# Kernel tuning notes

Measured on AMD Instinct MI355X. Metric: run time of the kernel, lower is better.

## Reference

```python
import jax, jax.numpy as jnp
import numpy as np

B, CIN, H, W = 16, 3, 128, 128
C = 256          # out_channels
NH = 8           # num_heads
HD = C // NH     # head_dim = 32
SCALE = HD ** -0.5
EPS = 1e-5


def setup_inputs() -> dict:
    key = jax.random.key(0)
    ks = jax.random.split(key, 8)
    def xavier(k, fan_out, fan_in):
        lim = np.sqrt(6.0 / (fan_in + fan_out))
        return jax.random.uniform(k, (fan_out, fan_in), jnp.float32, -lim, lim)
    return {
        "x": jax.random.normal(ks[0], (B, CIN, H, W), jnp.float32),
        "Wi": xavier(ks[1], C, CIN),      # input_conv 1x1
        "bi": jnp.zeros((C,), jnp.float32),
        "Wqkv": xavier(ks[2], 3 * C, C),  # qkv_conv 1x1, no bias
        "Wo": xavier(ks[3], C, C),        # output_proj
        "bo": jnp.zeros((C,), jnp.float32),
        "Wf": xavier(ks[4], C, C),        # feature_update_conv
        "bf": jnp.zeros((C,), jnp.float32),
        "gamma": jnp.ones((C,), jnp.float32),
        "beta": jnp.zeros((C,), jnp.float32),
        "rmean": jnp.zeros((C,), jnp.float32),
        "rvar": jnp.ones((C,), jnp.float32),
    }


def reference(x, Wi, bi, Wqkv, Wo, bo, Wf, bf, gamma, beta, rmean, rvar):
    b, _, h, w = x.shape
    hw = h * w
    # input 1x1 conv
    x1 = jnp.einsum('oi,bihw->bohw', Wi, x) + bi[:, None, None]
    # qkv 1x1 conv, reshape (b, NH, 3, HD, h*w) matching torch channel layout
    qkv = jnp.einsum('oi,bihw->bohw', Wqkv, x1).reshape(b, NH, 3, HD, hw)
    q, k, v = qkv[:, :, 0], qkv[:, :, 1], qkv[:, :, 2]  # each (b, NH, HD, hw)
    # channel-channel attention: (b, NH, HD, HD), sigmoid gate (no softmax)
    attention = jax.nn.sigmoid(jnp.einsum('bndp,bnep->bnde', q, k) * SCALE)
    A = jnp.einsum('bnde,bnep->bndp', attention, v).reshape(b, C, h, w)
    A = jnp.einsum('oi,bihw->bohw', Wo, A) + bo[:, None, None]
    A = jnp.einsum('oi,bihw->bohw', Wf, A) + bf[:, None, None]
    # BatchNorm2d (eval mode: running stats)
    inv = gamma / jnp.sqrt(rvar + EPS)
    A = (A - rmean[:, None, None]) * inv[:, None, None] + beta[:, None, None]
    A = jax.nn.silu(A)  # dropout is identity in eval
    out = A + x1
    return (out, attention)
```

## Files before the change

kernel.cpp:

```cpp
#include <hip/hip_runtime.h>
#include <math.h>


#define HW 16384
#define NBATCH 16
static constexpr float SCALE_ = 0.17677669529663687f;
static constexpr float EPS_ = 1e-5f;

#define WS_PART 0
#define WS_WFO  4096
#define WS_BFO  69632
#define WS_WB4  69888
#define WS_AQ   71168
#define WS_GG   76800

__device__ __forceinline__ float sigmoidf_(float z) {
  return 1.0f / (1.0f + __expf(-z));
}

__global__ __launch_bounds__(256) void k_prep(
    const float* __restrict__ x,
    const float* __restrict__ Wi, const float* __restrict__ bi,
    const float* __restrict__ Wqkv,
    const float* __restrict__ Wo, const float* __restrict__ bo,
    const float* __restrict__ Wf, const float* __restrict__ bf,
    float* __restrict__ part, float* __restrict__ Wfo,
    float* __restrict__ bfo, float* __restrict__ Wb4,
    float* __restrict__ aqg)
{
  const int bx = blockIdx.x;
  const int tid = threadIdx.x;
  if (bx < 256) {
    const int b = bx >> 4;
    const int pi = bx & 15;
    const int p0 = pi * 1024 + tid * 4;
    const float4 a0 = *reinterpret_cast<const float4*>(x + (size_t)(b * 3 + 0) * HW + p0);
    const float4 a1 = *reinterpret_cast<const float4*>(x + (size_t)(b * 3 + 1) * HW + p0);
    const float4 a2 = *reinterpret_cast<const float4*>(x + (size_t)(b * 3 + 2) * HW + p0);
    float v[9];
    v[0] = a0.x * a0.x + a0.y * a0.y + a0.z * a0.z + a0.w * a0.w;
    v[1] = a0.x * a1.x + a0.y * a1.y + a0.z * a1.z + a0.w * a1.w;
    v[2] = a0.x * a2.x + a0.y * a2.y + a0.z * a2.z + a0.w * a2.w;
    v[3] = a1.x * a1.x + a1.y * a1.y + a1.z * a1.z + a1.w * a1.w;
    v[4] = a1.x * a2.x + a1.y * a2.y + a1.z * a2.z + a1.w * a2.w;
    v[5] = a2.x * a2.x + a2.y * a2.y + a2.z * a2.z + a2.w * a2.w;
    v[6] = a0.x + a0.y + a0.z + a0.w;
    v[7] = a1.x + a1.y + a1.z + a1.w;
    v[8] = a2.x + a2.y + a2.z + a2.w;
    __shared__ float wred[4][9];
    const int lane = tid & 63, wid = tid >> 6;
#pragma unroll
    for (int k = 0; k < 9; ++k) {
      float s = v[k];
#pragma unroll
      for (int off = 32; off; off >>= 1) s += __shfl_down(s, off, 64);
      if (lane == 0) wred[wid][k] = s;
    }
    __syncthreads();
    if (tid < 9) {
      part[bx * 9 + tid] = wred[0][tid] + wred[1][tid] + wred[2][tid] + wred[3][tid];
    }
  } else if (bx < 512) {
    const int o = bx - 256;
    const float* wfr = Wf + (size_t)o * 256;
    const int i = tid;
    float acc = 0.f;
#pragma unroll 8
    for (int k = 0; k < 256; ++k) acc = fmaf(wfr[k], Wo[(size_t)k * 256 + i], acc);
    Wfo[(size_t)o * 256 + i] = acc;
  } else if (bx == 512) {
    Wb4[tid * 4 + 0] = Wi[tid * 3 + 0];
    Wb4[tid * 4 + 1] = Wi[tid * 3 + 1];
    Wb4[tid * 4 + 2] = Wi[tid * 3 + 2];
    Wb4[tid * 4 + 3] = bi[tid];
    float acc = bf[tid];
    const float* wfr = Wf + (size_t)tid * 256;
#pragma unroll 8
    for (int k = 0; k < 256; ++k) acc = fmaf(wfr[k], bo[k], acc);
    bfo[tid] = acc;
  } else {
    const int blk = bx - 513;
    const int rl = tid >> 2;
    const int ch = tid & 3;
    const int row = blk * 64 + rl;
    const float* wr = Wqkv + (size_t)row * 256 + ch * 64;
    float c0 = 0, c1 = 0, c2 = 0, c3 = 0;
#pragma unroll 8
    for (int c = 0; c < 64; ++c) {
      const float w = wr[c];
      const int cc = ch * 64 + c;
      c0 = fmaf(w, Wi[cc * 3 + 0], c0);
      c1 = fmaf(w, Wi[cc * 3 + 1], c1);
      c2 = fmaf(w, Wi[cc * 3 + 2], c2);
      c3 = fmaf(w, bi[cc], c3);
    }
    __shared__ float red[64][4][4];
    red[rl][ch][0] = c0; red[rl][ch][1] = c1;
    red[rl][ch][2] = c2; red[rl][ch][3] = c3;
    __syncthreads();
    const int j = tid & 3;
    aqg[(size_t)(blk * 64 + rl) * 4 + j] =
        red[rl][0][j] + red[rl][1][j] + red[rl][2][j] + red[rl][3][j];
  }
}

__global__ __launch_bounds__(1024) void k_solve(
    const float* __restrict__ part, const float* __restrict__ aqg,
    const float* __restrict__ Wfo, const float* __restrict__ bfo,
    const float* __restrict__ gamma, const float* __restrict__ beta,
    const float* __restrict__ rmean, const float* __restrict__ rvar,
    float* __restrict__ att_out,
    float* __restrict__ Gg)
{
  const int b = blockIdx.x;
  const int tid = threadIdx.x;
  __shared__ float Ms[9];
  __shared__ float aq[768][5];
  __shared__ float att_s[8][32][33];
  __shared__ float4 A4[256];
  __shared__ float4 redv[256][4];

  if (tid < 9) {
    float s = 0.f;
    for (int j = 0; j < 16; ++j) s += part[(b * 16 + j) * 9 + tid];
    Ms[tid] = s;
  }
  for (int i = tid; i < 3072; i += 1024) aq[i >> 2][i & 3] = aqg[i];
  __syncthreads();
  const float M00 = Ms[0], M01 = Ms[1], M02 = Ms[2], M11 = Ms[3], M12 = Ms[4], M22 = Ms[5];
  const float s0 = Ms[6], s1 = Ms[7], s2 = Ms[8];
  for (int idx = tid; idx < 8192; idx += 1024) {
    const int n = idx >> 10, r = idx & 1023, d = r >> 5, e = r & 31;
    const float* q = aq[n * 96 + d];
    const float* k = aq[n * 96 + 32 + e];
    const float q0 = q[0], q1 = q[1], q2 = q[2], q3 = q[3];
    const float k0 = k[0], k1 = k[1], k2 = k[2], k3 = k[3];
    const float t = q0 * (M00 * k0 + M01 * k1 + M02 * k2)
                  + q1 * (M01 * k0 + M11 * k1 + M12 * k2)
                  + q2 * (M02 * k0 + M12 * k1 + M22 * k2)
                  + q3 * (s0 * k0 + s1 * k1 + s2 * k2)
                  + k3 * (s0 * q0 + s1 * q1 + s2 * q2)
                  + 16384.0f * q3 * k3;
    const float a = sigmoidf_(SCALE_ * t);
    att_s[n][d][e] = a;
    att_out[b * 8192 + idx] = a;
  }
  __syncthreads();
  {
    const int c = tid >> 2, j = tid & 3;
    const int n = c >> 5, d = c & 31;
    float acc = 0.f;
    const float* arow = att_s[n][d];
#pragma unroll 8
    for (int e = 0; e < 32; ++e) acc = fmaf(arow[e], aq[n * 96 + 64 + e][j], acc);
    ((float*)&A4[c])[j] = acc;
  }
  __syncthreads();
  {
    const int o = tid >> 2, ch = tid & 3;
    const float* wr = Wfo + (size_t)o * 256 + ch * 64;
    float a0 = 0, a1 = 0, a2 = 0, a3 = 0;
#pragma unroll 8
    for (int i = 0; i < 64; ++i) {
      const float w = wr[i];
      const float4 av = A4[ch * 64 + i];
      a0 = fmaf(w, av.x, a0);
      a1 = fmaf(w, av.y, a1);
      a2 = fmaf(w, av.z, a2);
      a3 = fmaf(w, av.w, a3);
    }
    redv[o][ch] = make_float4(a0, a1, a2, a3);
  }
  __syncthreads();
  {
    const int o = tid >> 2, j = tid & 3;
    float acc = ((const float*)&redv[o][0])[j] + ((const float*)&redv[o][1])[j]
              + ((const float*)&redv[o][2])[j] + ((const float*)&redv[o][3])[j];
    if (j == 3) acc += bfo[o];
    const float inv = gamma[o] / sqrtf(rvar[o] + EPS_);
    float outv;
    if (j == 3) outv = (acc - rmean[o]) * inv + beta[o];
    else        outv = acc * inv;
    Gg[(size_t)(b * 256 + o) * 4 + j] = outv;
  }
}

__global__ __launch_bounds__(256) void k_final(
    const float* __restrict__ x,
    const float4* __restrict__ Gg4,
    const float4* __restrict__ Wb4,
    float* __restrict__ out)
{
  const int b = blockIdx.z;
  const int c0 = blockIdx.y * 32;
  const int tid = threadIdx.x;
  const int p4 = (blockIdx.x * 256 + tid) * 4;
  __shared__ float4 sg[32], sw[32];
  if (tid < 32) sg[tid] = Gg4[b * 256 + c0 + tid];
  else if (tid < 64) sw[tid - 32] = Wb4[c0 + tid - 32];
  __syncthreads();
  const float4 X0 = *reinterpret_cast<const float4*>(x + (size_t)(b * 3 + 0) * HW + p4);
  const float4 X1 = *reinterpret_cast<const float4*>(x + (size_t)(b * 3 + 1) * HW + p4);
  const float4 X2 = *reinterpret_cast<const float4*>(x + (size_t)(b * 3 + 2) * HW + p4);
  float* ob = out + (size_t)(b * 256 + c0) * HW + p4;
#pragma unroll 2
  for (int ci = 0; ci < 32; ++ci) {
    const float4 g = sg[ci];
    const float4 w = sw[ci];
    float4 r;
    {
      const float y = fmaf(g.x, X0.x, fmaf(g.y, X1.x, fmaf(g.z, X2.x, g.w)));
      const float sil = y * sigmoidf_(y);
      r.x = sil + fmaf(w.x, X0.x, fmaf(w.y, X1.x, fmaf(w.z, X2.x, w.w)));
    }
    {
      const float y = fmaf(g.x, X0.y, fmaf(g.y, X1.y, fmaf(g.z, X2.y, g.w)));
      const float sil = y * sigmoidf_(y);
      r.y = sil + fmaf(w.x, X0.y, fmaf(w.y, X1.y, fmaf(w.z, X2.y, w.w)));
    }
    {
      const float y = fmaf(g.x, X0.z, fmaf(g.y, X1.z, fmaf(g.z, X2.z, g.w)));
      const float sil = y * sigmoidf_(y);
      r.z = sil + fmaf(w.x, X0.z, fmaf(w.y, X1.z, fmaf(w.z, X2.z, w.w)));
    }
    {
      const float y = fmaf(g.x, X0.w, fmaf(g.y, X1.w, fmaf(g.z, X2.w, g.w)));
      const float sil = y * sigmoidf_(y);
      r.w = sil + fmaf(w.x, X0.w, fmaf(w.y, X1.w, fmaf(w.z, X2.w, w.w)));
    }
    *reinterpret_cast<float4*>(ob) = r;
    ob += HW;
  }
}

extern "C" void kernel_launch(void* const* d_in, const int* in_sizes, int n_in,
                              void* d_out, int out_size, void* d_ws, size_t ws_size,
                              hipStream_t stream) {
  const float* x     = (const float*)d_in[0];
  const float* Wi    = (const float*)d_in[1];
  const float* bi    = (const float*)d_in[2];
  const float* Wqkv  = (const float*)d_in[3];
  const float* Wo    = (const float*)d_in[4];
  const float* bo    = (const float*)d_in[5];
  const float* Wf    = (const float*)d_in[6];
  const float* bf    = (const float*)d_in[7];
  const float* gamma = (const float*)d_in[8];
  const float* beta  = (const float*)d_in[9];
  const float* rmean = (const float*)d_in[10];
  const float* rvar  = (const float*)d_in[11];

  float* out = (float*)d_out;
  float* att = out + (size_t)NBATCH * 256 * HW;
  float* wsf = (float*)d_ws;

  k_prep<<<dim3(525), dim3(256), 0, stream>>>(x, Wi, bi, Wqkv, Wo, bo, Wf, bf,
                                              wsf + WS_PART, wsf + WS_WFO,
                                              wsf + WS_BFO, wsf + WS_WB4,
                                              wsf + WS_AQ);
  k_solve<<<dim3(NBATCH), dim3(1024), 0, stream>>>(wsf + WS_PART, wsf + WS_AQ,
                                                   wsf + WS_WFO, wsf + WS_BFO,
                                                   gamma, beta, rmean, rvar,
                                                   att, wsf + WS_GG);
  k_final<<<dim3(16, 8, NBATCH), dim3(256), 0, stream>>>(
      x, (const float4*)(wsf + WS_GG), (const float4*)(wsf + WS_WB4), out);
}
```

Before: 80.49 us.

## Split solve kernel per head and fuse output projection into final kernel

Replaces the 16-block per-batch solve kernel with a per-(head,batch) kernel that computes the sigmoid channel attention and attention·v. The Wfo projection, bias and batchnorm folding move into the prologue of the final elementwise kernel, computed per 32-channel slice. This spreads the serial solve stage across many more CUs to cut its latency. In exchange, every final block redundantly loads a 32x256 Wfo slice and does a small reduction before streaming output. Some prep-loop unroll factors are also raised.

```diff
diff --git a/kernel.cpp b/kernel.cpp
--- a/kernel.cpp
+++ b/kernel.cpp
@@ -12,7 +12,7 @@
 #define WS_BFO  69632
 #define WS_WB4  69888
 #define WS_AQ   71168
-#define WS_GG   76800
+#define WS_A4G  75776
 
 __device__ __forceinline__ float sigmoidf_(float z) {
   return 1.0f / (1.0f + __expf(-z));
@@ -65,7 +65,7 @@
     const float* wfr = Wf + (size_t)o * 256;
     const int i = tid;
     float acc = 0.f;
-#pragma unroll 8
+#pragma unroll 32
     for (int k = 0; k < 256; ++k) acc = fmaf(wfr[k], Wo[(size_t)k * 256 + i], acc);
     Wfo[(size_t)o * 256 + i] = acc;
   } else if (bx == 512) {
@@ -75,7 +75,7 @@
     Wb4[tid * 4 + 3] = bi[tid];
     float acc = bf[tid];
     const float* wfr = Wf + (size_t)tid * 256;
-#pragma unroll 8
+#pragma unroll 16
     for (int k = 0; k < 256; ++k) acc = fmaf(wfr[k], bo[k], acc);
     bfo[tid] = acc;
   } else {
@@ -104,35 +104,35 @@
   }
 }
 
-__global__ __launch_bounds__(1024) void k_solve(
+__global__ __launch_bounds__(256) void k_solveA(
     const float* __restrict__ part, const float* __restrict__ aqg,
-    const float* __restrict__ Wfo, const float* __restrict__ bfo,
-    const float* __restrict__ gamma, const float* __restrict__ beta,
-    const float* __restrict__ rmean, const float* __restrict__ rvar,
     float* __restrict__ att_out,
-    float* __restrict__ Gg)
+    float* __restrict__ A4g)
 {
-  const int b = blockIdx.x;
+  const int n = blockIdx.x;
+  const int b = blockIdx.y;
   const int tid = threadIdx.x;
   __shared__ float Ms[9];
-  __shared__ float aq[768][5];
-  __shared__ float att_s[8][32][33];
-  __shared__ float4 A4[256];
-  __shared__ float4 redv[256][4];
-
+  __shared__ float aqh[96][5];
+  __shared__ float att_s[32][33];
   if (tid < 9) {
     float s = 0.f;
     for (int j = 0; j < 16; ++j) s += part[(b * 16 + j) * 9 + tid];
     Ms[tid] = s;
   }
-  for (int i = tid; i < 3072; i += 1024) aq[i >> 2][i & 3] = aqg[i];
+  if (tid < 96) {
+    const float4 v = *reinterpret_cast<const float4*>(aqg + (size_t)(n * 96 + tid) * 4);
+    aqh[tid][0] = v.x; aqh[tid][1] = v.y; aqh[tid][2] = v.z; aqh[tid][3] = v.w;
+  }
   __syncthreads();
   const float M00 = Ms[0], M01 = Ms[1], M02 = Ms[2], M11 = Ms[3], M12 = Ms[4], M22 = Ms[5];
   const float s0 = Ms[6], s1 = Ms[7], s2 = Ms[8];
-  for (int idx = tid; idx < 8192; idx += 1024) {
-    const int n = idx >> 10, r = idx & 1023, d = r >> 5, e = r & 31;
-    const float* q = aq[n * 96 + d];
-    const float* k = aq[n * 96 + 32 + e];
+#pragma unroll
+  for (int r = 0; r < 4; ++r) {
+    const int idx = tid + r * 256;
+    const int d = idx >> 5, e = idx & 31;
+    const float* q = aqh[d];
+    const float* k = aqh[32 + e];
     const float q0 = q[0], q1 = q[1], q2 = q[2], q3 = q[3];
     const float k0 = k[0], k1 = k[1], k2 = k[2], k3 = k[3];
     const float t = q0 * (M00 * k0 + M01 * k1 + M02 * k2)
@@ -142,91 +142,101 @@
                   + k3 * (s0 * q0 + s1 * q1 + s2 * q2)
                   + 16384.0f * q3 * k3;
     const float a = sigmoidf_(SCALE_ * t);
-    att_s[n][d][e] = a;
-    att_out[b * 8192 + idx] = a;
-  }
-  __syncthreads();
-  {
-    const int c = tid >> 2, j = tid & 3;
-    const int n = c >> 5, d = c & 31;
+    att_s[d][e] = a;
+    att_out[(size_t)(b * 8 + n) * 1024 + idx] = a;
+  }
+  __syncthreads();
+  if (tid < 128) {
+    const int d = tid >> 2, j = tid & 3;
     float acc = 0.f;
-    const float* arow = att_s[n][d];
 #pragma unroll 8
-    for (int e = 0; e < 32; ++e) acc = fmaf(arow[e], aq[n * 96 + 64 + e][j], acc);
-    ((float*)&A4[c])[j] = acc;
-  }
-  __syncthreads();
-  {
-    const int o = tid >> 2, ch = tid & 3;
-    const float* wr = Wfo + (size_t)o * 256 + ch * 64;
-    float a0 = 0, a1 = 0, a2 = 0, a3 = 0;
-#pragma unroll 8
-    for (int i = 0; i < 64; ++i) {
-      const float w = wr[i];
-      const float4 av = A4[ch * 64 + i];
-      a0 = fmaf(w, av.x, a0);
-      a1 = fmaf(w, av.y, a1);
-      a2 = fmaf(w, av.z, a2);
-      a3 = fmaf(w, av.w, a3);
-    }
-    redv[o][ch] = make_float4(a0, a1, a2, a3);
-  }
-  __syncthreads();
-  {
-    const int o = tid >> 2, j = tid & 3;
-    float acc = ((const float*)&redv[o][0])[j] + ((const float*)&redv[o][1])[j]
-              + ((const float*)&redv[o][2])[j] + ((const float*)&redv[o][3])[j];
-    if (j == 3) acc += bfo[o];
-    const float inv = gamma[o] / sqrtf(rvar[o] + EPS_);
-    float outv;
-    if (j == 3) outv = (acc - rmean[o]) * inv + beta[o];
-    else        outv = acc * inv;
-    Gg[(size_t)(b * 256 + o) * 4 + j] = outv;
+    for (int e = 0; e < 32; ++e) acc = fmaf(att_s[d][e], aqh[64 + e][j], acc);
+    A4g[(size_t)(b * 256 + n * 32 + d) * 4 + j] = acc;
   }
 }
 
 __global__ __launch_bounds__(256) void k_final(
     const float* __restrict__ x,
-    const float4* __restrict__ Gg4,
-    const float4* __restrict__ Wb4,
+    const float* __restrict__ Wfo, const float* __restrict__ bfo,
+    const float* __restrict__ A4g, const float4* __restrict__ Wb4,
+    const float* __restrict__ gamma, const float* __restrict__ beta,
+    const float* __restrict__ rmean, const float* __restrict__ rvar,
     float* __restrict__ out)
 {
   const int b = blockIdx.z;
   const int c0 = blockIdx.y * 32;
   const int tid = threadIdx.x;
+  __shared__ float4 A4v[256];
+  __shared__ float Wfo_s[32][257];
+  __shared__ float4 partial[32][9];
+  __shared__ float4 gg_s[32];
+  __shared__ float4 wb_s[32];
+
+  A4v[tid] = *reinterpret_cast<const float4*>(A4g + ((size_t)b * 256 + tid) * 4);
+#pragma unroll
+  for (int it = 0; it < 8; ++it) {
+    const int idx = tid + it * 256;
+    const int r = idx >> 6, kq = idx & 63;
+    const float4 v = *reinterpret_cast<const float4*>(
+        Wfo + ((size_t)(c0 + r) * 256 + kq * 4));
+    Wfo_s[r][kq * 4 + 0] = v.x; Wfo_s[r][kq * 4 + 1] = v.y;
+    Wfo_s[r][kq * 4 + 2] = v.z; Wfo_s[r][kq * 4 + 3] = v.w;
+  }
+  __syncthreads();
+  {
+    const int ks = tid >> 5, o = tid & 31;
+    float4 acc = make_float4(0.f, 0.f, 0.f, 0.f);
+#pragma unroll 8
+    for (int i = 0; i < 32; ++i) {
+      const float w = Wfo_s[o][ks * 32 + i];
+      const float4 a = A4v[ks * 32 + i];
+      acc.x = fmaf(w, a.x, acc.x); acc.y = fmaf(w, a.y, acc.y);
+      acc.z = fmaf(w, a.z, acc.z); acc.w = fmaf(w, a.w, acc.w);
+    }
+    partial[o][ks] = acc;
+  }
+  __syncthreads();
+  if (tid < 32) {
+    const int o = tid;
+    float4 s = partial[o][0];
+#pragma unroll
+    for (int k2 = 1; k2 < 8; ++k2) {
+      const float4 p = partial[o][k2];
+      s.x += p.x; s.y += p.y; s.z += p.z; s.w += p.w;
+    }
+    const int c = c0 + o;
+    const float inv = gamma[c] / sqrtf(rvar[c] + EPS_);
+    const float g3 = (s.w + bfo[c] - rmean[c]) * inv + beta[c];
+    gg_s[o] = make_float4(s.x * inv, s.y * inv, s.z * inv, g3);
+    wb_s[o] = Wb4[c];
+  }
+  __syncthreads();
+
   const int p4 = (blockIdx.x * 256 + tid) * 4;
-  __shared__ float4 sg[32], sw[32];
-  if (tid < 32) sg[tid] = Gg4[b * 256 + c0 + tid];
-  else if (tid < 64) sw[tid - 32] = Wb4[c0 + tid - 32];
-  __syncthreads();
   const float4 X0 = *reinterpret_cast<const float4*>(x + (size_t)(b * 3 + 0) * HW + p4);
   const float4 X1 = *reinterpret_cast<const float4*>(x + (size_t)(b * 3 + 1) * HW + p4);
   const float4 X2 = *reinterpret_cast<const float4*>(x + (size_t)(b * 3 + 2) * HW + p4);
   float* ob = out + (size_t)(b * 256 + c0) * HW + p4;
 #pragma unroll 2
   for (int ci = 0; ci < 32; ++ci) {
-    const float4 g = sg[ci];
-    const float4 w = sw[ci];
+    const float4 g = gg_s[ci];
+    const float4 w = wb_s[ci];
     float4 r;
     {
       const float y = fmaf(g.x, X0.x, fmaf(g.y, X1.x, fmaf(g.z, X2.x, g.w)));
-      const float sil = y * sigmoidf_(y);
-      r.x = sil + fmaf(w.x, X0.x, fmaf(w.y, X1.x, fmaf(w.z, X2.x, w.w)));
+      r.x = y * sigmoidf_(y) + fmaf(w.x, X0.x, fmaf(w.y, X1.x, fmaf(w.z, X2.x, w.w)));
     }
     {
       const float y = fmaf(g.x, X0.y, fmaf(g.y, X1.y, fmaf(g.z, X2.y, g.w)));
-      const float sil = y * sigmoidf_(y);
-      r.y = sil + fmaf(w.x, X0.y, fmaf(w.y, X1.y, fmaf(w.z, X2.y, w.w)));
+      r.y = y * sigmoidf_(y) + fmaf(w.x, X0.y, fmaf(w.y, X1.y, fmaf(w.z, X2.y, w.w)));
     }
     {
       const float y = fmaf(g.x, X0.z, fmaf(g.y, X1.z, fmaf(g.z, X2.z, g.w)));
-      const float sil = y * sigmoidf_(y);
-      r.z = sil + fmaf(w.x, X0.z, fmaf(w.y, X1.z, fmaf(w.z, X2.z, w.w)));
+      r.z = y * sigmoidf_(y) + fmaf(w.x, X0.z, fmaf(w.y, X1.z, fmaf(w.z, X2.z, w.w)));
     }
     {
       const float y = fmaf(g.x, X0.w, fmaf(g.y, X1.w, fmaf(g.z, X2.w, g.w)));
-      const float sil = y * sigmoidf_(y);
-      r.w = sil + fmaf(w.x, X0.w, fmaf(w.y, X1.w, fmaf(w.z, X2.w, w.w)));
+      r.w = y * sigmoidf_(y) + fmaf(w.x, X0.w, fmaf(w.y, X1.w, fmaf(w.z, X2.w, w.w)));
     }
     *reinterpret_cast<float4*>(ob) = r;
     ob += HW;
@@ -257,10 +267,9 @@
                                               wsf + WS_PART, wsf + WS_WFO,
                                               wsf + WS_BFO, wsf + WS_WB4,
                                               wsf + WS_AQ);
-  k_solve<<<dim3(NBATCH), dim3(1024), 0, stream>>>(wsf + WS_PART, wsf + WS_AQ,
-                                                   wsf + WS_WFO, wsf + WS_BFO,
-                                                   gamma, beta, rmean, rvar,
-                                                   att, wsf + WS_GG);
+  k_solveA<<<dim3(8, NBATCH), dim3(256), 0, stream>>>(wsf + WS_PART, wsf + WS_AQ,
+                                                      att, wsf + WS_A4G);
   k_final<<<dim3(16, 8, NBATCH), dim3(256), 0, stream>>>(
-      x, (const float4*)(wsf + WS_GG), (const float4*)(wsf + WS_WB4), out);
-}
+      x, wsf + WS_WFO, wsf + WS_BFO, wsf + WS_A4G,
+      (const float4*)(wsf + WS_WB4), gamma, beta, rmean, rvar, out);
+}
```

After: 70.69 us. 12.2% less time.
